# Kernel optimization log

Hardware: AMD Instinct MI355X
Metric: run time of the kernel (lower is better)

The kernel has to match this reference:

```python
import jax, jax.numpy as jnp
import numpy as np

N = 100000   # graph nodes (TSP edges)
E = 600000   # graph edges
IN_DIM = 2; HID = 128; HEADS = 16; DH = HID // HEADS
L = 4; FF = 2 * HID; OUT = 1
EPS = 1e-5; SLOPE = 0.2  # BatchNorm eps, GAT leaky_relu slope


def _mlp(x, W1, b1, W2, b2):
    return jnp.maximum(x @ W1 + b1, 0.0) @ W2 + b2


def _bn(x, g, b):
    # BatchNorm1d in training mode: batch (node-dim) statistics, biased variance
    mu = x.mean(0)
    var = x.var(0)
    return (x - mu) * jax.lax.rsqrt(var + EPS) * g + b


def _gat(h, src, dst, W, al, ar, bias):
    # DGL GATConv: per-head projection, additive attention, edge softmax over incoming edges
    z = (h @ W).reshape(N, HEADS, DH)          # [N,H,Dh]
    el = (z * al).sum(-1)                      # [N,H] source term
    er = (z * ar).sum(-1)                      # [N,H] dest term
    e = jax.nn.leaky_relu(el[src] + er[dst], SLOPE)            # [E,H]
    m = jax.ops.segment_max(e, dst, num_segments=N)            # [N,H]
    a = jnp.exp(e - m[dst])                                    # [E,H]
    denom = jax.ops.segment_sum(a, dst, num_segments=N)        # [N,H]
    msg = jax.ops.segment_sum(a[:, :, None] * z[src], dst, num_segments=N)  # [N,H,Dh]
    out = msg / jnp.where(denom > 0, denom, 1.0)[:, :, None]
    return out.reshape(N, HID) + bias


def _forward(x, src, dst,
             emb_W1, emb_b1, emb_W2, emb_b2, emb_Ws, emb_bs,
             gat_W, gat_al, gat_ar, gat_b, bn1_g, bn1_b,
             ff_W1, ff_b1, ff_W2, ff_b2, bn2_g, bn2_b,
             dec_W1, dec_b1, dec_W2, dec_b2):
    # embed MLP with skip connection
    h = _mlp(x, emb_W1, emb_b1, emb_W2, emb_b2) + (x @ emb_Ws + emb_bs)
    xs = [h]
    for l in range(L):  # fixed small layer count
        a = _gat(h, src, dst, gat_W[l], gat_al[l], gat_ar[l], gat_b[l])
        h = _bn(h + a, bn1_g[l], bn1_b[l])
        f = _mlp(h, ff_W1[l], ff_b1[l], ff_W2[l], ff_b2[l])
        h = _bn(h + f, bn2_g[l], bn2_b[l])
        xs.append(h)
    hc = jnp.concatenate(xs, axis=-1)  # JumpingKnowledge 'cat' -> [N, HID*(L+1)]
    return _mlp(hc, dec_W1, dec_b1, dec_W2, dec_b2)


def setup_inputs() -> dict:
    key = jax.random.key(0)
    ks = jax.random.split(key, 20)
    w = lambda k, shape: jax.random.normal(k, shape, jnp.float32) * 0.05
    x = jax.random.normal(ks[0], (N, IN_DIM), jnp.float32)
    src = jax.random.randint(ks[1], (E,), 0, N)
    # guarantee every node has at least one incoming edge
    dst = jnp.concatenate([jnp.arange(N), jax.random.randint(ks[2], (E - N,), 0, N)])
    return {
        'x': x, 'src': src, 'dst': dst,
        'emb_W1': w(ks[3], (IN_DIM, HID)), 'emb_b1': jnp.zeros((HID,), jnp.float32),
        'emb_W2': w(ks[4], (HID, HID)),    'emb_b2': jnp.zeros((HID,), jnp.float32),
        'emb_Ws': w(ks[5], (IN_DIM, HID)), 'emb_bs': jnp.zeros((HID,), jnp.float32),
        'gat_W': w(ks[6], (L, HID, HID)),
        'gat_al': w(ks[7], (L, HEADS, DH)), 'gat_ar': w(ks[8], (L, HEADS, DH)),
        'gat_b': jnp.zeros((L, HID), jnp.float32),
        'bn1_g': jnp.ones((L, HID), jnp.float32), 'bn1_b': jnp.zeros((L, HID), jnp.float32),
        'ff_W1': w(ks[9], (L, HID, FF)),  'ff_b1': jnp.zeros((L, FF), jnp.float32),
        'ff_W2': w(ks[10], (L, FF, HID)), 'ff_b2': jnp.zeros((L, HID), jnp.float32),
        'bn2_g': jnp.ones((L, HID), jnp.float32), 'bn2_b': jnp.zeros((L, HID), jnp.float32),
        'dec_W1': w(ks[11], (HID * (L + 1), HID)), 'dec_b1': jnp.zeros((HID,), jnp.float32),
        'dec_W2': w(ks[12], (HID, OUT)),           'dec_b2': jnp.zeros((OUT,), jnp.float32),
    }


def reference(x, src, dst,
              emb_W1, emb_b1, emb_W2, emb_b2, emb_Ws, emb_bs,
              gat_W, gat_al, gat_ar, gat_b, bn1_g, bn1_b,
              ff_W1, ff_b1, ff_W2, ff_b2, bn2_g, bn2_b,
              dec_W1, dec_b1, dec_W2, dec_b2):
    return _forward(x, src, dst,
                    emb_W1, emb_b1, emb_W2, emb_b2, emb_Ws, emb_bs,
                    gat_W, gat_al, gat_ar, gat_b, bn1_g, bn1_b,
                    ff_W1, ff_b1, ff_W2, ff_b2, bn2_g, bn2_b,
                    dec_W1, dec_b1, dec_W2, dec_b2)
```

## Files before the change

### kernel.cpp

```cpp
#include <hip/hip_runtime.h>
#include <math.h>

typedef __attribute__((ext_vector_type(8))) short bf16x8;
typedef __attribute__((ext_vector_type(4))) float f32x4;

struct BN5 {
    const float* st[5];
    const float* g[5];
    const float* b[5];
    const float* stR;
    const float* gR;
    const float* bR;
    float invN;
};

static __device__ __forceinline__ short f2bf(float f) {
    unsigned u = __float_as_uint(f);
    unsigned r = (u + 0x7fffu + ((u >> 16) & 1u)) >> 16;
    return (short)r;
}
static __device__ __forceinline__ float bf2f(short s) {
    return __uint_as_float(((unsigned)(unsigned short)s) << 16);
}
static __device__ __forceinline__ float bflo(int v) { return bf2f((short)(v & 0xffff)); }
static __device__ __forceinline__ float bfhi(int v) { return bf2f((short)(((unsigned)v) >> 16)); }
static __device__ __forceinline__ int pack2(float a, float b) {
    return (int)(((unsigned)(unsigned short)f2bf(b) << 16) | (unsigned)(unsigned short)f2bf(a));
}

__global__ void zero_i32_k(int* __restrict__ p, int n) {
    int i = blockIdx.x * 256 + threadIdx.x;
    if (i < n) p[i] = 0;
}

__global__ __launch_bounds__(256) void wconv_k(const float* __restrict__ W, short* __restrict__ Wt,
                                               int K, int Nc) {
    int slice = blockIdx.y;
    const float* src = W + (size_t)slice * K * Nc;
    short* dst = Wt + (size_t)slice * K * Nc;
    int idx = blockIdx.x * 256 + threadIdx.x;
    if (idx >= K * Nc) return;
    int k = idx / Nc, n = idx - k * Nc;
    dst[(size_t)n * K + k] = f2bf(src[idx]);
}

__global__ __launch_bounds__(256) void embed_k(
    const float* __restrict__ x, const float* __restrict__ W1, const float* __restrict__ b1,
    const float* __restrict__ Ws, const float* __restrict__ bs,
    int* __restrict__ u2, int* __restrict__ h2, int Nn)
{
    int idx = blockIdx.x * 256 + threadIdx.x;
    if (idx >= Nn * 64) return;
    int n = idx >> 6, c = (idx & 63) * 2;
    float x0 = x[2*n], x1 = x[2*n+1];
    float u0 = fmaxf(fmaf(x1, W1[128+c],   fmaf(x0, W1[c],   b1[c])),   0.f);
    float u1 = fmaxf(fmaf(x1, W1[128+c+1], fmaf(x0, W1[c+1], b1[c+1])), 0.f);
    float h0 = fmaf(x1, Ws[128+c],   fmaf(x0, Ws[c],   bs[c]));
    float h1 = fmaf(x1, Ws[128+c+1], fmaf(x0, Ws[c+1], bs[c+1]));
    u2[idx] = pack2(u0, u1);
    h2[idx] = pack2(h0, h1);
}

template<int NK, int RELU, int BETA, int ELR, int STATS>
__global__ __launch_bounds__(256) void gemm2_k(
    const short* __restrict__ A0, const short* __restrict__ A1,
    const short* __restrict__ A2, const short* __restrict__ A3,
    const short* __restrict__ A4, int Astr,
    const short* __restrict__ Wt, int ldWt,
    const float* __restrict__ bias, short* __restrict__ C, const short* __restrict__ Rres,
    int Nrows, int ldC, BN5 bn,
    const float* __restrict__ al, const float* __restrict__ ar,
    float* __restrict__ elo, float* __restrict__ ero,
    float* __restrict__ statsOut)
{
    __shared__ short Bs[128][136];
    const int row0 = blockIdx.x * 128;
    const int col0 = blockIdx.y * 128;
    const int t = threadIdx.x;
    const int w = t >> 6, lane = t & 63, q = lane >> 4, m = lane & 15;

    f32x4 acc[2][8];
    #pragma unroll
    for (int rb = 0; rb < 2; ++rb)
        #pragma unroll
        for (int cb = 0; cb < 8; ++cb)
            acc[rb][cb] = (f32x4){0.f, 0.f, 0.f, 0.f};

    const short* Asrc[5] = {A0, A1, A2, A3, A4};
    int rr0 = row0 + w*32 + m;      if (rr0 > Nrows - 1) rr0 = Nrows - 1;
    int rr1 = row0 + w*32 + 16 + m; if (rr1 > Nrows - 1) rr1 = Nrows - 1;

    #pragma unroll
    for (int kh = 0; kh < NK; ++kh) {
        if (kh) __syncthreads();
        #pragma unroll
        for (int it = 0; it < 8; ++it) {
            int ci = t + it * 256;
            int r = ci >> 4, j = (ci & 15) * 8;
            *(int4*)&Bs[r][j] = *(const int4*)(Wt + (size_t)(col0 + r) * ldWt + kh * 128 + j);
        }
        const short* pa0 = Asrc[kh] + (size_t)rr0 * Astr + q * 8;
        const short* pa1 = Asrc[kh] + (size_t)rr1 * Astr + q * 8;
        bf16x8 af0[4], af1[4];
        #pragma unroll
        for (int ks = 0; ks < 4; ++ks) {
            af0[ks] = *(const bf16x8*)(pa0 + ks * 32);
            af1[ks] = *(const bf16x8*)(pa1 + ks * 32);
        }
        if (bn.st[kh]) {
            const float* st = bn.st[kh];
            const float* gg = bn.g[kh];
            const float* bb = bn.b[kh];
            #pragma unroll
            for (int ks = 0; ks < 4; ++ks) {
                #pragma unroll
                for (int e = 0; e < 8; ++e) {
                    int c = ks * 32 + q * 8 + e;
                    float mu = st[c] * bn.invN;
                    float var = st[128 + c] * bn.invN - mu * mu;
                    float sc = rsqrtf(var + 1e-5f) * gg[c];
                    float bc = bb[c] - mu * sc;
                    af0[ks][e] = f2bf(fmaf(bf2f(af0[ks][e]), sc, bc));
                    af1[ks][e] = f2bf(fmaf(bf2f(af1[ks][e]), sc, bc));
                }
            }
        }
        __syncthreads();
        #pragma unroll
        for (int ks = 0; ks < 4; ++ks) {
            bf16x8 bfr[8];
            #pragma unroll
            for (int cb = 0; cb < 8; ++cb)
                bfr[cb] = *(const bf16x8*)&Bs[cb * 16 + m][ks * 32 + q * 8];
            #pragma unroll
            for (int cb = 0; cb < 8; ++cb) {
                acc[0][cb] = __builtin_amdgcn_mfma_f32_16x16x32_bf16(af0[ks], bfr[cb], acc[0][cb], 0, 0, 0);
                acc[1][cb] = __builtin_amdgcn_mfma_f32_16x16x32_bf16(af1[ks], bfr[cb], acc[1][cb], 0, 0, 0);
            }
        }
    }

    __syncthreads();
    short* Cs = (short*)Bs;
    #pragma unroll
    for (int rb = 0; rb < 2; ++rb) {
        #pragma unroll
        for (int r = 0; r < 4; ++r) {
            int lrow = w * 32 + rb * 16 + q * 4 + r;
            #pragma unroll
            for (int cb = 0; cb < 8; ++cb) {
                float v = acc[rb][cb][r];
                if (bias) v += bias[col0 + cb * 16 + m];
                if (RELU) v = fmaxf(v, 0.f);
                Cs[lrow * 132 + cb * 16 + m] = f2bf(v);
            }
        }
    }
    __syncthreads();
    const int chunk = t & 15, rgrp = t >> 4, cb8 = chunk * 8;
    const short* Rd = Rres ? Rres : C;
    float scR[8], bbR[8];
    if (BETA) {
        if (bn.stR) {
            #pragma unroll
            for (int e = 0; e < 8; ++e) {
                int c = cb8 + e;
                float mu = bn.stR[c] * bn.invN;
                float var = bn.stR[128 + c] * bn.invN - mu * mu;
                float sc = rsqrtf(var + 1e-5f) * bn.gR[c];
                scR[e] = sc; bbR[e] = bn.bR[c] - mu * sc;
            }
        }
    }
    float sS[8], sQ[8];
    if (STATS) {
        #pragma unroll
        for (int e = 0; e < 8; ++e) { sS[e] = 0.f; sQ[e] = 0.f; }
    }
    #pragma unroll
    for (int j = 0; j < 8; ++j) {
        int r = rgrp + j * 16;
        int grow = row0 + r;
        if (grow < Nrows) {
            int2 u0 = *(const int2*)(Cs + r * 132 + cb8);
            int2 u1 = *(const int2*)(Cs + r * 132 + cb8 + 4);
            int4 cv = make_int4(u0.x, u0.y, u1.x, u1.y);
            size_t gb = (size_t)grow * ldC + col0 + cb8;
            if (BETA) {
                int4 rv = *(const int4*)(Rd + gb);
                int* cp = (int*)&cv; const int* rp = (const int*)&rv;
                #pragma unroll
                for (int e = 0; e < 4; ++e) {
                    float rlo = bflo(rp[e]), rhi = bfhi(rp[e]);
                    if (bn.stR) {
                        rlo = fmaf(rlo, scR[2*e],   bbR[2*e]);
                        rhi = fmaf(rhi, scR[2*e+1], bbR[2*e+1]);
                    }
                    cp[e] = pack2(bflo(cp[e]) + rlo, bfhi(cp[e]) + rhi);
                }
            }
            *(int4*)(C + gb) = cv;
            if (ELR) {
                const int* cp = (const int*)&cv;
                float sl = 0.f, sr = 0.f;
                #pragma unroll
                for (int e = 0; e < 4; ++e) {
                    float lo = bflo(cp[e]), hi = bfhi(cp[e]);
                    sl = fmaf(lo, al[cb8 + 2*e], sl); sl = fmaf(hi, al[cb8 + 2*e + 1], sl);
                    sr = fmaf(lo, ar[cb8 + 2*e], sr); sr = fmaf(hi, ar[cb8 + 2*e + 1], sr);
                }
                elo[(size_t)grow * 16 + chunk] = sl;
                ero[(size_t)grow * 16 + chunk] = sr;
            }
            if (STATS) {
                const int* cp = (const int*)&cv;
                #pragma unroll
                for (int e = 0; e < 4; ++e) {
                    float lo = bflo(cp[e]), hi = bfhi(cp[e]);
                    sS[2*e]   += lo; sQ[2*e]   += lo * lo;
                    sS[2*e+1] += hi; sQ[2*e+1] += hi * hi;
                }
            }
        }
    }
    if (STATS) {
        __syncthreads();
        float* fs = (float*)Bs;
        #pragma unroll
        for (int e = 0; e < 8; ++e) {
            fs[rgrp * 128 + cb8 + e]        = sS[e];
            fs[2048 + rgrp * 128 + cb8 + e] = sQ[e];
        }
        __syncthreads();
        if (t < 128) {
            float a = 0.f;
            #pragma unroll
            for (int g = 0; g < 16; ++g) a += fs[g * 128 + t];
            atomicAdd(&statsOut[t], a);
        } else {
            int c = t - 128;
            float a = 0.f;
            #pragma unroll
            for (int g = 0; g < 16; ++g) a += fs[2048 + g * 128 + c];
            atomicAdd(&statsOut[128 + c], a);
        }
    }
}

__global__ void count_k(const int* __restrict__ dst, int* __restrict__ cnt, int E) {
    int e = blockIdx.x * 256 + threadIdx.x;
    if (e < E) atomicAdd(&cnt[dst[e]], 1);
}

__global__ __launch_bounds__(256) void scan_part_k(const int* __restrict__ cnt,
                                                   int* __restrict__ bsum, int Nn) {
    __shared__ int red[256];
    int base = blockIdx.x * 1024;
    int s = 0;
    for (int i = threadIdx.x; i < 1024; i += 256) {
        int g = base + i;
        if (g < Nn) s += cnt[g];
    }
    red[threadIdx.x] = s; __syncthreads();
    for (int off = 128; off; off >>= 1) {
        if ((int)threadIdx.x < off) red[threadIdx.x] += red[threadIdx.x + off];
        __syncthreads();
    }
    if (threadIdx.x == 0) bsum[blockIdx.x] = red[0];
}

__global__ __launch_bounds__(256) void scan_top_k(int* __restrict__ bsum, int nb) {
    __shared__ int buf[256];
    int v = ((int)threadIdx.x < nb) ? bsum[threadIdx.x] : 0;
    buf[threadIdx.x] = v; __syncthreads();
    for (int off = 1; off < 256; off <<= 1) {
        int tv = ((int)threadIdx.x >= off) ? buf[threadIdx.x - off] : 0;
        __syncthreads();
        buf[threadIdx.x] += tv;
        __syncthreads();
    }
    if ((int)threadIdx.x < nb) bsum[threadIdx.x] = buf[threadIdx.x] - v;
}

__global__ __launch_bounds__(256) void scan_fin_k(const int* __restrict__ cnt,
    const int* __restrict__ bsum, int* __restrict__ rowptr, int* __restrict__ wpos, int Nn)
{
    __shared__ int tsum[256];
    int base = blockIdx.x * 1024;
    int g0 = base + (int)threadIdx.x * 4;
    int v[4]; int s = 0;
    #pragma unroll
    for (int j = 0; j < 4; ++j) {
        int g = g0 + j;
        v[j] = (g < Nn) ? cnt[g] : 0;
        s += v[j];
    }
    tsum[threadIdx.x] = s; __syncthreads();
    for (int off = 1; off < 256; off <<= 1) {
        int tv = ((int)threadIdx.x >= off) ? tsum[threadIdx.x - off] : 0;
        __syncthreads();
        tsum[threadIdx.x] += tv;
        __syncthreads();
    }
    int run = bsum[blockIdx.x] + tsum[threadIdx.x] - s;
    #pragma unroll
    for (int j = 0; j < 4; ++j) {
        int g = g0 + j;
        if (g < Nn) { wpos[g] = run; rowptr[g + 1] = run + v[j]; }
        run += v[j];
    }
    if (blockIdx.x == 0 && threadIdx.x == 0) rowptr[0] = 0;
}

__global__ void scatter_k(const int* __restrict__ src, const int* __restrict__ dst,
                          int* __restrict__ wpos, int* __restrict__ esrc, int E) {
    int e = blockIdx.x * 256 + threadIdx.x;
    if (e < E) {
        int p = atomicAdd(&wpos[dst[e]], 1);
        esrc[p] = src[e];
    }
}

__global__ __launch_bounds__(256) void gat_k(
    const short* __restrict__ h, const short* __restrict__ z,
    const float* __restrict__ el, const float* __restrict__ er,
    const int* __restrict__ rowptr, const int* __restrict__ esrc,
    const float* __restrict__ gbias, short* __restrict__ t1, int Nn,
    const float* __restrict__ hstats, const float* __restrict__ hg,
    const float* __restrict__ hb, float invN)
{
    int gw = (blockIdx.x * 256 + threadIdx.x) >> 6;
    if (gw >= Nn) return;
    int lane = threadIdx.x & 63;
    int c = lane * 2;
    int head = lane >> 2;
    float ern = er[gw*16 + head];
    int beg = rowptr[gw], end = rowptr[gw+1];
    float m = -3.0e38f, den = 0.f, a0 = 0.f, a1 = 0.f;
    int i = beg;
    for (; i + 3 < end; i += 4) {
        int s0 = esrc[i], s1 = esrc[i+1], s2 = esrc[i+2], s3 = esrc[i+3];
        float e0 = el[s0*16 + head] + ern;
        float e1 = el[s1*16 + head] + ern;
        float e2 = el[s2*16 + head] + ern;
        float e3 = el[s3*16 + head] + ern;
        int zz0 = *(const int*)(z + (size_t)s0*128 + c);
        int zz1 = *(const int*)(z + (size_t)s1*128 + c);
        int zz2 = *(const int*)(z + (size_t)s2*128 + c);
        int zz3 = *(const int*)(z + (size_t)s3*128 + c);
        e0 = (e0 > 0.f) ? e0 : 0.2f * e0;
        e1 = (e1 > 0.f) ? e1 : 0.2f * e1;
        e2 = (e2 > 0.f) ? e2 : 0.2f * e2;
        e3 = (e3 > 0.f) ? e3 : 0.2f * e3;
        float nm = fmaxf(fmaxf(fmaxf(e0, e1), fmaxf(e2, e3)), m);
        float sc = __expf(m - nm);
        float w0 = __expf(e0 - nm), w1 = __expf(e1 - nm);
        float w2 = __expf(e2 - nm), w3 = __expf(e3 - nm);
        den = fmaf(den, sc, (w0 + w1) + (w2 + w3));
        a0 = fmaf(a0, sc, fmaf(w0, bflo(zz0), fmaf(w1, bflo(zz1), fmaf(w2, bflo(zz2), w3 * bflo(zz3)))));
        a1 = fmaf(a1, sc, fmaf(w0, bfhi(zz0), fmaf(w1, bfhi(zz1), fmaf(w2, bfhi(zz2), w3 * bfhi(zz3)))));
        m = nm;
    }
    for (; i + 1 < end; i += 2) {
        int s0 = esrc[i], s1 = esrc[i+1];
        float e0 = el[s0*16 + head] + ern;
        float e1 = el[s1*16 + head] + ern;
        int zz0 = *(const int*)(z + (size_t)s0*128 + c);
        int zz1 = *(const int*)(z + (size_t)s1*128 + c);
        e0 = (e0 > 0.f) ? e0 : 0.2f * e0;
        e1 = (e1 > 0.f) ? e1 : 0.2f * e1;
        float nm = fmaxf(m, fmaxf(e0, e1));
        float sc = __expf(m - nm);
        float w0 = __expf(e0 - nm);
        float w1 = __expf(e1 - nm);
        den = fmaf(den, sc, w0 + w1);
        a0  = fmaf(a0, sc, fmaf(w0, bflo(zz0), w1 * bflo(zz1)));
        a1  = fmaf(a1, sc, fmaf(w0, bfhi(zz0), w1 * bfhi(zz1)));
        m = nm;
    }
    if (i < end) {
        int s0 = esrc[i];
        float e0 = el[s0*16 + head] + ern;
        int zz0 = *(const int*)(z + (size_t)s0*128 + c);
        e0 = (e0 > 0.f) ? e0 : 0.2f * e0;
        float nm = fmaxf(m, e0);
        float sc = __expf(m - nm);
        float w0 = __expf(e0 - nm);
        den = fmaf(den, sc, w0);
        a0  = fmaf(a0, sc, w0 * bflo(zz0));
        a1  = fmaf(a1, sc, w0 * bfhi(zz0));
    }
    float inv = 1.f / den;
    size_t o = (size_t)gw*64 + lane;
    int hv = ((const int*)h)[o];
    float h0 = bflo(hv), h1 = bfhi(hv);
    if (hstats) {
        float mu0 = hstats[c] * invN;
        float v0  = hstats[128+c] * invN - mu0*mu0;
        float s0  = rsqrtf(v0 + 1e-5f) * hg[c];
        h0 = fmaf(h0 - mu0, s0, hb[c]);
        float mu1 = hstats[c+1] * invN;
        float v1  = hstats[128+c+1] * invN - mu1*mu1;
        float s1  = rsqrtf(v1 + 1e-5f) * hg[c+1];
        h1 = fmaf(h1 - mu1, s1, hb[c+1]);
    }
    float r0 = h0 + a0*inv + gbias[c];
    float r1 = h1 + a1*inv + gbias[c+1];
    ((int*)t1)[o] = pack2(r0, r1);
}

__global__ __launch_bounds__(256) void bn_stats_k(const short* __restrict__ xin,
    float* __restrict__ stats, int Nn)
{
    __shared__ float s0s[256], s1s[256], q0s[256], q1s[256];
    int pair = threadIdx.x & 63;
    int slot = threadIdx.x >> 6;
    float s0 = 0.f, s1 = 0.f, q0 = 0.f, q1 = 0.f;
    for (int r = blockIdx.x*4 + slot; r < Nn; r += gridDim.x*4) {
        int v = *(const int*)(xin + (size_t)r*128 + pair*2);
        float a = bflo(v), b = bfhi(v);
        s0 += a; s1 += b;
        q0 = fmaf(a, a, q0); q1 = fmaf(b, b, q1);
    }
    s0s[threadIdx.x] = s0; s1s[threadIdx.x] = s1;
    q0s[threadIdx.x] = q0; q1s[threadIdx.x] = q1;
    __syncthreads();
    if (slot == 0) {
        #pragma unroll
        for (int j = 1; j < 4; ++j) {
            s0 += s0s[pair + j*64]; s1 += s1s[pair + j*64];
            q0 += q0s[pair + j*64]; q1 += q1s[pair + j*64];
        }
        atomicAdd(&stats[pair*2],       s0);
        atomicAdd(&stats[pair*2+1],     s1);
        atomicAdd(&stats[128+pair*2],   q0);
        atomicAdd(&stats[128+pair*2+1], q1);
    }
}

__global__ __launch_bounds__(256) void dec_out_k(const short* __restrict__ udec,
    const float* __restrict__ W2, const float* __restrict__ b2,
    float* __restrict__ out, int Nn)
{
    int gw = (blockIdx.x * 256 + threadIdx.x) >> 6;
    if (gw >= Nn) return;
    int lane = threadIdx.x & 63;
    int v = ((const int*)(udec + (size_t)gw * 128))[lane];
    float p = bflo(v) * W2[lane*2] + bfhi(v) * W2[lane*2 + 1];
    #pragma unroll
    for (int off = 32; off > 0; off >>= 1) p += __shfl_down(p, off);
    if (lane == 0) out[gw] = p + b2[0];
}

extern "C" void kernel_launch(void* const* d_in, const int* in_sizes, int n_in,
                              void* d_out, int out_size, void* d_ws, size_t ws_size,
                              hipStream_t stream)
{
    const float* x      = (const float*)d_in[0];
    const int*   src    = (const int*)  d_in[1];
    const int*   dst    = (const int*)  d_in[2];
    const float* emb_W1 = (const float*)d_in[3];
    const float* emb_b1 = (const float*)d_in[4];
    const float* emb_W2 = (const float*)d_in[5];
    const float* emb_b2 = (const float*)d_in[6];
    const float* emb_Ws = (const float*)d_in[7];
    const float* emb_bs = (const float*)d_in[8];
    const float* gat_W  = (const float*)d_in[9];
    const float* gat_al = (const float*)d_in[10];
    const float* gat_ar = (const float*)d_in[11];
    const float* gat_b  = (const float*)d_in[12];
    const float* bn1_g  = (const float*)d_in[13];
    const float* bn1_b  = (const float*)d_in[14];
    const float* ff_W1  = (const float*)d_in[15];
    const float* ff_b1  = (const float*)d_in[16];
    const float* ff_W2  = (const float*)d_in[17];
    const float* ff_b2  = (const float*)d_in[18];
    const float* bn2_g  = (const float*)d_in[19];
    const float* bn2_b  = (const float*)d_in[20];
    const float* dec_W1 = (const float*)d_in[21];
    const float* dec_b1 = (const float*)d_in[22];
    const float* dec_W2 = (const float*)d_in[23];
    const float* dec_b2 = (const float*)d_in[24];
    float* out = (float*)d_out;
    (void)n_in; (void)out_size;

    const int N = in_sizes[0] / 2;
    const int E = in_sizes[1];
    const float invN = 1.f / (float)N;

    char* p = (char*)d_ws;
    size_t used = 0;
    auto carve = [&](size_t bytes) {
        char* r = p; size_t a = (bytes + 255) & ~(size_t)255;
        p += a; used += a; return r;
    };
    const size_t nbH = (size_t)N * 128 * 2;
    short* xs[5];
    for (int i = 0; i < 5; ++i) xs[i] = (short*)carve(nbH);
    short* t1   = (short*)carve(nbH);
    char*  big  = (char*)carve(2 * nbH);
    int*   cnt    = (int*)carve((size_t)N * 4);
    float* stats8 = (float*)carve(8 * 256 * 4);
    int*   rowptr = (int*)carve((size_t)(N + 1) * 4);
    int*   wpos   = (int*)carve((size_t)N * 4);
    int*   esrc   = (int*)carve((size_t)E * 4);
    int*   bsum   = (int*)carve(256 * 4);
    short* emb_W2t = (short*)carve((size_t)128 * 128 * 2);
    short* gat_Wt  = (short*)carve((size_t)4 * 128 * 128 * 2);
    short* ff_W1t  = (short*)carve((size_t)4 * 128 * 256 * 2);
    short* ff_W2t  = (short*)carve((size_t)4 * 256 * 128 * 2);
    short* dec_W1t = (short*)carve((size_t)640 * 128 * 2);
    if (used > ws_size) return;

    short* u    = (short*)big;
    short* z    = (short*)big;
    float* el   = (float*)(big + nbH);
    float* er   = el + (size_t)N * 16;
    short* ffh  = (short*)big;
    short* udec = (short*)big;

    dim3 b256(256);
    int ecb  = (E + 255) / 256;
    int nel2 = (N * 64 + 255) / 256;
    int gx   = (N + 127) / 128;
    int nwv  = (N + 3) / 4;
    int nb   = (N + 1023) / 1024;

    BN5 bn0;
    for (int i = 0; i < 5; ++i) { bn0.st[i] = nullptr; bn0.g[i] = nullptr; bn0.b[i] = nullptr; }
    bn0.stR = nullptr; bn0.gR = nullptr; bn0.bR = nullptr; bn0.invN = invN;

    wconv_k<<<dim3(64, 1), b256, 0, stream>>>(emb_W2, emb_W2t, 128, 128);
    wconv_k<<<dim3(64, 4), b256, 0, stream>>>(gat_W,  gat_Wt,  128, 128);
    wconv_k<<<dim3(128, 4), b256, 0, stream>>>(ff_W1, ff_W1t,  128, 256);
    wconv_k<<<dim3(128, 4), b256, 0, stream>>>(ff_W2, ff_W2t,  256, 128);
    wconv_k<<<dim3(320, 1), b256, 0, stream>>>(dec_W1, dec_W1t, 640, 128);

    {
        int ztot = (int)(((char*)(stats8 + 8*256) - (char*)cnt) / 4);
        zero_i32_k<<<(ztot + 255) / 256, b256, 0, stream>>>(cnt, ztot);
    }

    count_k<<<ecb, b256, 0, stream>>>(dst, cnt, E);
    scan_part_k<<<nb, b256, 0, stream>>>(cnt, bsum, N);
    scan_top_k<<<1, b256, 0, stream>>>(bsum, nb);
    scan_fin_k<<<nb, b256, 0, stream>>>(cnt, bsum, rowptr, wpos, N);
    scatter_k<<<ecb, b256, 0, stream>>>(src, dst, wpos, esrc, E);

    embed_k<<<nel2, b256, 0, stream>>>(x, emb_W1, emb_b1, emb_Ws, emb_bs, (int*)u, (int*)xs[0], N);
    gemm2_k<1,0,1,0,0><<<dim3(gx,1), b256, 0, stream>>>(u,u,u,u,u, 128, emb_W2t, 128,
        emb_b2, xs[0], nullptr, N, 128, bn0, nullptr, nullptr, nullptr, nullptr, nullptr);

    for (int l = 0; l < 4; ++l) {
        float* st1 = stats8 + (size_t)(l*2)   * 256;
        float* st2 = stats8 + (size_t)(l*2+1) * 256;
        short* hl = xs[l];
        const float* hst = (l == 0) ? nullptr : stats8 + (size_t)((l-1)*2+1) * 256;
        const float* hgp = (l == 0) ? nullptr : bn2_g + (l-1)*128;
        const float* hbp = (l == 0) ? nullptr : bn2_b + (l-1)*128;

        BN5 bz = bn0; bz.st[0] = hst; bz.g[0] = hgp; bz.b[0] = hbp;
        gemm2_k<1,0,0,1,0><<<dim3(gx,1), b256, 0, stream>>>(hl,hl,hl,hl,hl, 128,
            gat_Wt + (size_t)l*128*128, 128, nullptr, z, nullptr, N, 128, bz,
            gat_al + l*128, gat_ar + l*128, el, er, nullptr);
        gat_k<<<nwv, b256, 0, stream>>>(hl, z, el, er, rowptr, esrc, gat_b + l*128, t1, N,
                                        hst, hgp, hbp, invN);
        bn_stats_k<<<400, b256, 0, stream>>>(t1, st1, N);
        BN5 bf1 = bn0; bf1.st[0] = st1; bf1.g[0] = bn1_g + l*128; bf1.b[0] = bn1_b + l*128;
        gemm2_k<1,1,0,0,0><<<dim3(gx,2), b256, 0, stream>>>(t1,t1,t1,t1,t1, 128,
            ff_W1t + (size_t)l*128*256, 128, ff_b1 + l*256, ffh, nullptr, N, 256, bf1,
            nullptr, nullptr, nullptr, nullptr, nullptr);
        BN5 bf2 = bn0; bf2.stR = st1; bf2.gR = bn1_g + l*128; bf2.bR = bn1_b + l*128;
        gemm2_k<2,0,1,0,1><<<dim3(gx,1), b256, 0, stream>>>(ffh, ffh + 128, ffh, ffh, ffh, 256,
            ff_W2t + (size_t)l*256*128, 256, ff_b2 + l*128, xs[l+1], t1, N, 128, bf2,
            nullptr, nullptr, nullptr, nullptr, st2);
    }

    BN5 bd = bn0;
    for (int k = 1; k < 5; ++k) {
        bd.st[k] = stats8 + (size_t)((k-1)*2+1) * 256;
        bd.g[k]  = bn2_g + (k-1)*128;
        bd.b[k]  = bn2_b + (k-1)*128;
    }
    gemm2_k<5,1,0,0,0><<<dim3(gx,1), b256, 0, stream>>>(xs[0], xs[1], xs[2], xs[3], xs[4], 128,
        dec_W1t, 640, dec_b1, udec, nullptr, N, 128, bd,
        nullptr, nullptr, nullptr, nullptr, nullptr);
    dec_out_k<<<nwv, b256, 0, stream>>>(udec, dec_W2, dec_b2, out, N);
}
```

Measured before the change: 1.146 ms.

## Fuse feed-forward MLP GEMMs into one kernel keeping hidden activations in LDS

Replaces the two FF GEMM launches per layer with a single kernel. It applies BN1 to the input rows, computes the 256-wide ReLU hidden layer in two 128-column halves held in shared memory, and accumulates the second GEMM directly. The residual add, BN2 statistics and output store move into the same epilogue. This drops the N×256 bf16 hidden-activation round trip through global memory and one launch per layer. In exchange it uses more shared memory per block, holds more accumulator registers and adds extra syncthreads, which may lower occupancy.

New measurement: 1.062 ms. -7.4%, faster.

```diff
diff --git a/kernel.cpp b/kernel.cpp
--- a/kernel.cpp
+++ b/kernel.cpp
@@ -61,7 +61,7 @@
     h2[idx] = pack2(h0, h1);
 }
 
-template<int NK, int RELU, int BETA, int ELR, int STATS>
+template<int NK, int RELU, int BETA, int ELR>
 __global__ __launch_bounds__(256) void gemm2_k(
     const short* __restrict__ A0, const short* __restrict__ A1,
     const short* __restrict__ A2, const short* __restrict__ A3,
@@ -70,8 +70,7 @@
     const float* __restrict__ bias, short* __restrict__ C, const short* __restrict__ Rres,
     int Nrows, int ldC, BN5 bn,
     const float* __restrict__ al, const float* __restrict__ ar,
-    float* __restrict__ elo, float* __restrict__ ero,
-    float* __restrict__ statsOut)
+    float* __restrict__ elo, float* __restrict__ ero)
 {
     __shared__ short Bs[128][136];
     const int row0 = blockIdx.x * 128;
@@ -159,24 +158,6 @@
     __syncthreads();
     const int chunk = t & 15, rgrp = t >> 4, cb8 = chunk * 8;
     const short* Rd = Rres ? Rres : C;
-    float scR[8], bbR[8];
-    if (BETA) {
-        if (bn.stR) {
-            #pragma unroll
-            for (int e = 0; e < 8; ++e) {
-                int c = cb8 + e;
-                float mu = bn.stR[c] * bn.invN;
-                float var = bn.stR[128 + c] * bn.invN - mu * mu;
-                float sc = rsqrtf(var + 1e-5f) * bn.gR[c];
-                scR[e] = sc; bbR[e] = bn.bR[c] - mu * sc;
-            }
-        }
-    }
-    float sS[8], sQ[8];
-    if (STATS) {
-        #pragma unroll
-        for (int e = 0; e < 8; ++e) { sS[e] = 0.f; sQ[e] = 0.f; }
-    }
     #pragma unroll
     for (int j = 0; j < 8; ++j) {
         int r = rgrp + j * 16;
@@ -190,14 +171,8 @@
                 int4 rv = *(const int4*)(Rd + gb);
                 int* cp = (int*)&cv; const int* rp = (const int*)&rv;
                 #pragma unroll
-                for (int e = 0; e < 4; ++e) {
-                    float rlo = bflo(rp[e]), rhi = bfhi(rp[e]);
-                    if (bn.stR) {
-                        rlo = fmaf(rlo, scR[2*e],   bbR[2*e]);
-                        rhi = fmaf(rhi, scR[2*e+1], bbR[2*e+1]);
-                    }
-                    cp[e] = pack2(bflo(cp[e]) + rlo, bfhi(cp[e]) + rhi);
-                }
+                for (int e = 0; e < 4; ++e)
+                    cp[e] = pack2(bflo(cp[e]) + bflo(rp[e]), bfhi(cp[e]) + bfhi(rp[e]));
             }
             *(int4*)(C + gb) = cv;
             if (ELR) {
@@ -212,38 +187,195 @@
                 elo[(size_t)grow * 16 + chunk] = sl;
                 ero[(size_t)grow * 16 + chunk] = sr;
             }
-            if (STATS) {
-                const int* cp = (const int*)&cv;
+        }
+    }
+}
+
+__global__ __launch_bounds__(256) void ff_fused_k(
+    const short* __restrict__ T1,
+    const short* __restrict__ W1t,
+    const short* __restrict__ W2t,
+    const float* __restrict__ b1, const float* __restrict__ b2,
+    const float* __restrict__ st1, const float* __restrict__ g1, const float* __restrict__ bb1,
+    float invN, short* __restrict__ C, int Nrows, float* __restrict__ statsOut)
+{
+    __shared__ short Wbuf[128][136];
+    __shared__ short Fbuf[128 * 132];
+    const int row0 = blockIdx.x * 128;
+    const int t = threadIdx.x;
+    const int w = t >> 6, lane = t & 63, q = lane >> 4, m = lane & 15;
+
+    f32x4 acc2[2][8];
+    #pragma unroll
+    for (int rb = 0; rb < 2; ++rb)
+        #pragma unroll
+        for (int cb = 0; cb < 8; ++cb)
+            acc2[rb][cb] = (f32x4){0.f, 0.f, 0.f, 0.f};
+
+    int rr0 = row0 + w*32 + m;      if (rr0 > Nrows - 1) rr0 = Nrows - 1;
+    int rr1 = row0 + w*32 + 16 + m; if (rr1 > Nrows - 1) rr1 = Nrows - 1;
+
+    bf16x8 af0[4], af1[4];
+    {
+        const short* pa0 = T1 + (size_t)rr0 * 128 + q * 8;
+        const short* pa1 = T1 + (size_t)rr1 * 128 + q * 8;
+        #pragma unroll
+        for (int ks = 0; ks < 4; ++ks) {
+            af0[ks] = *(const bf16x8*)(pa0 + ks * 32);
+            af1[ks] = *(const bf16x8*)(pa1 + ks * 32);
+        }
+        #pragma unroll
+        for (int ks = 0; ks < 4; ++ks) {
+            #pragma unroll
+            for (int e = 0; e < 8; ++e) {
+                int c = ks * 32 + q * 8 + e;
+                float mu = st1[c] * invN;
+                float var = st1[128 + c] * invN - mu * mu;
+                float sc = rsqrtf(var + 1e-5f) * g1[c];
+                float bc = bb1[c] - mu * sc;
+                af0[ks][e] = f2bf(fmaf(bf2f(af0[ks][e]), sc, bc));
+                af1[ks][e] = f2bf(fmaf(bf2f(af1[ks][e]), sc, bc));
+            }
+        }
+    }
+
+    #pragma unroll
+    for (int half = 0; half < 2; ++half) {
+        if (half) __syncthreads();
+        #pragma unroll
+        for (int it = 0; it < 8; ++it) {
+            int ci = t + it * 256;
+            int r = ci >> 4, j = (ci & 15) * 8;
+            *(int4*)&Wbuf[r][j] = *(const int4*)(W1t + (size_t)(half * 128 + r) * 128 + j);
+        }
+        __syncthreads();
+        f32x4 acc1[2][8];
+        #pragma unroll
+        for (int rb = 0; rb < 2; ++rb)
+            #pragma unroll
+            for (int cb = 0; cb < 8; ++cb)
+                acc1[rb][cb] = (f32x4){0.f, 0.f, 0.f, 0.f};
+        #pragma unroll
+        for (int ks = 0; ks < 4; ++ks) {
+            bf16x8 bfr[8];
+            #pragma unroll
+            for (int cb = 0; cb < 8; ++cb)
+                bfr[cb] = *(const bf16x8*)&Wbuf[cb * 16 + m][ks * 32 + q * 8];
+            #pragma unroll
+            for (int cb = 0; cb < 8; ++cb) {
+                acc1[0][cb] = __builtin_amdgcn_mfma_f32_16x16x32_bf16(af0[ks], bfr[cb], acc1[0][cb], 0, 0, 0);
+                acc1[1][cb] = __builtin_amdgcn_mfma_f32_16x16x32_bf16(af1[ks], bfr[cb], acc1[1][cb], 0, 0, 0);
+            }
+        }
+        #pragma unroll
+        for (int rb = 0; rb < 2; ++rb) {
+            #pragma unroll
+            for (int r = 0; r < 4; ++r) {
+                int lrow = w * 32 + rb * 16 + q * 4 + r;
                 #pragma unroll
-                for (int e = 0; e < 4; ++e) {
-                    float lo = bflo(cp[e]), hi = bfhi(cp[e]);
-                    sS[2*e]   += lo; sQ[2*e]   += lo * lo;
-                    sS[2*e+1] += hi; sQ[2*e+1] += hi * hi;
+                for (int cb = 0; cb < 8; ++cb) {
+                    float v = acc1[rb][cb][r] + b1[half * 128 + cb * 16 + m];
+                    Fbuf[lrow * 132 + cb * 16 + m] = f2bf(fmaxf(v, 0.f));
                 }
             }
         }
-    }
-    if (STATS) {
-        __syncthreads();
-        float* fs = (float*)Bs;
-        #pragma unroll
-        for (int e = 0; e < 8; ++e) {
-            fs[rgrp * 128 + cb8 + e]        = sS[e];
-            fs[2048 + rgrp * 128 + cb8 + e] = sQ[e];
-        }
-        __syncthreads();
-        if (t < 128) {
-            float a = 0.f;
-            #pragma unroll
-            for (int g = 0; g < 16; ++g) a += fs[g * 128 + t];
-            atomicAdd(&statsOut[t], a);
-        } else {
-            int c = t - 128;
-            float a = 0.f;
-            #pragma unroll
-            for (int g = 0; g < 16; ++g) a += fs[2048 + g * 128 + c];
-            atomicAdd(&statsOut[128 + c], a);
-        }
+        __syncthreads();
+        #pragma unroll
+        for (int it = 0; it < 8; ++it) {
+            int ci = t + it * 256;
+            int r = ci >> 4, j = (ci & 15) * 8;
+            *(int4*)&Wbuf[r][j] = *(const int4*)(W2t + (size_t)r * 256 + half * 128 + j);
+        }
+        __syncthreads();
+        const short* fa0 = Fbuf + (w * 32 + m) * 132 + q * 8;
+        const short* fa1 = Fbuf + (w * 32 + 16 + m) * 132 + q * 8;
+        #pragma unroll
+        for (int ks = 0; ks < 4; ++ks) {
+            bf16x8 ga0 = *(const bf16x8*)(fa0 + ks * 32);
+            bf16x8 ga1 = *(const bf16x8*)(fa1 + ks * 32);
+            bf16x8 bfr[8];
+            #pragma unroll
+            for (int cb = 0; cb < 8; ++cb)
+                bfr[cb] = *(const bf16x8*)&Wbuf[cb * 16 + m][ks * 32 + q * 8];
+            #pragma unroll
+            for (int cb = 0; cb < 8; ++cb) {
+                acc2[0][cb] = __builtin_amdgcn_mfma_f32_16x16x32_bf16(ga0, bfr[cb], acc2[0][cb], 0, 0, 0);
+                acc2[1][cb] = __builtin_amdgcn_mfma_f32_16x16x32_bf16(ga1, bfr[cb], acc2[1][cb], 0, 0, 0);
+            }
+        }
+    }
+
+    __syncthreads();
+    #pragma unroll
+    for (int rb = 0; rb < 2; ++rb) {
+        #pragma unroll
+        for (int r = 0; r < 4; ++r) {
+            int lrow = w * 32 + rb * 16 + q * 4 + r;
+            #pragma unroll
+            for (int cb = 0; cb < 8; ++cb) {
+                float v = acc2[rb][cb][r] + b2[cb * 16 + m];
+                Fbuf[lrow * 132 + cb * 16 + m] = f2bf(v);
+            }
+        }
+    }
+    __syncthreads();
+    const int chunk = t & 15, rgrp = t >> 4, cb8 = chunk * 8;
+    float scR[8], bbR[8];
+    #pragma unroll
+    for (int e = 0; e < 8; ++e) {
+        int c = cb8 + e;
+        float mu = st1[c] * invN;
+        float var = st1[128 + c] * invN - mu * mu;
+        float sc = rsqrtf(var + 1e-5f) * g1[c];
+        scR[e] = sc; bbR[e] = bb1[c] - mu * sc;
+    }
+    float sS[8], sQ[8];
+    #pragma unroll
+    for (int e = 0; e < 8; ++e) { sS[e] = 0.f; sQ[e] = 0.f; }
+    #pragma unroll
+    for (int j = 0; j < 8; ++j) {
+        int r = rgrp + j * 16;
+        int grow = row0 + r;
+        if (grow < Nrows) {
+            int2 u0 = *(const int2*)(Fbuf + r * 132 + cb8);
+            int2 u1 = *(const int2*)(Fbuf + r * 132 + cb8 + 4);
+            int4 cv = make_int4(u0.x, u0.y, u1.x, u1.y);
+            size_t gb = (size_t)grow * 128 + cb8;
+            int4 rv = *(const int4*)(T1 + gb);
+            int* cp = (int*)&cv; const int* rp = (const int*)&rv;
+            #pragma unroll
+            for (int e = 0; e < 4; ++e) {
+                float rlo = fmaf(bflo(rp[e]), scR[2*e],   bbR[2*e]);
+                float rhi = fmaf(bfhi(rp[e]), scR[2*e+1], bbR[2*e+1]);
+                float lo = bflo(cp[e]) + rlo;
+                float hi = bfhi(cp[e]) + rhi;
+                cp[e] = pack2(lo, hi);
+                lo = bflo(cp[e]); hi = bfhi(cp[e]);
+                sS[2*e]   += lo; sQ[2*e]   += lo * lo;
+                sS[2*e+1] += hi; sQ[2*e+1] += hi * hi;
+            }
+            *(int4*)(C + gb) = cv;
+        }
+    }
+    __syncthreads();
+    float* fs = (float*)Wbuf;
+    #pragma unroll
+    for (int e = 0; e < 8; ++e) {
+        fs[rgrp * 128 + cb8 + e]        = sS[e];
+        fs[2048 + rgrp * 128 + cb8 + e] = sQ[e];
+    }
+    __syncthreads();
+    if (t < 128) {
+        float a = 0.f;
+        #pragma unroll
+        for (int g = 0; g < 16; ++g) a += fs[g * 128 + t];
+        atomicAdd(&statsOut[t], a);
+    } else {
+        int c = t - 128;
+        float a = 0.f;
+        #pragma unroll
+        for (int g = 0; g < 16; ++g) a += fs[2048 + g * 128 + c];
+        atomicAdd(&statsOut[128 + c], a);
     }
 }
 
@@ -516,7 +648,6 @@
     short* z    = (short*)big;
     float* el   = (float*)(big + nbH);
     float* er   = el + (size_t)N * 16;
-    short* ffh  = (short*)big;
     short* udec = (short*)big;
 
     dim3 b256(256);
@@ -548,8 +679,8 @@
     scatter_k<<<ecb, b256, 0, stream>>>(src, dst, wpos, esrc, E);
 
     embed_k<<<nel2, b256, 0, stream>>>(x, emb_W1, emb_b1, emb_Ws, emb_bs, (int*)u, (int*)xs[0], N);
-    gemm2_k<1,0,1,0,0><<<dim3(gx,1), b256, 0, stream>>>(u,u,u,u,u, 128, emb_W2t, 128,
-        emb_b2, xs[0], nullptr, N, 128, bn0, nullptr, nullptr, nullptr, nullptr, nullptr);
+    gemm2_k<1,0,1,0><<<dim3(gx,1), b256, 0, stream>>>(u,u,u,u,u, 128, emb_W2t, 128,
+        emb_b2, xs[0], nullptr, N, 128, bn0, nullptr, nullptr, nullptr, nullptr);
 
     for (int l = 0; l < 4; ++l) {
         float* st1 = stats8 + (size_t)(l*2)   * 256;
@@ -560,20 +691,17 @@
         const float* hbp = (l == 0) ? nullptr : bn2_b + (l-1)*128;
 
         BN5 bz = bn0; bz.st[0] = hst; bz.g[0] = hgp; bz.b[0] = hbp;
-        gemm2_k<1,0,0,1,0><<<dim3(gx,1), b256, 0, stream>>>(hl,hl,hl,hl,hl, 128,
+        gemm2_k<1,0,0,1><<<dim3(gx,1), b256, 0, stream>>>(hl,hl,hl,hl,hl, 128,
             gat_Wt + (size_t)l*128*128, 128, nullptr, z, nullptr, N, 128, bz,
-            gat_al + l*128, gat_ar + l*128, el, er, nullptr);
+            gat_al + l*128, gat_ar + l*128, el, er);
         gat_k<<<nwv, b256, 0, stream>>>(hl, z, el, er, rowptr, esrc, gat_b + l*128, t1, N,
                                         hst, hgp, hbp, invN);
         bn_stats_k<<<400, b256, 0, stream>>>(t1, st1, N);
-        BN5 bf1 = bn0; bf1.st[0] = st1; bf1.g[0] = bn1_g + l*128; bf1.b[0] = bn1_b + l*128;
-        gemm2_k<1,1,0,0,0><<<dim3(gx,2), b256, 0, stream>>>(t1,t1,t1,t1,t1, 128,
-            ff_W1t + (size_t)l*128*256, 128, ff_b1 + l*256, ffh, nullptr, N, 256, bf1,
-            nullptr, nullptr, nullptr, nullptr, nullptr);
-        BN5 bf2 = bn0; bf2.stR = st1; bf2.gR = bn1_g + l*128; bf2.bR = bn1_b + l*128;
-        gemm2_k<2,0,1,0,1><<<dim3(gx,1), b256, 0, stream>>>(ffh, ffh + 128, ffh, ffh, ffh, 256,
-            ff_W2t + (size_t)l*256*128, 256, ff_b2 + l*128, xs[l+1], t1, N, 128, bf2,
-            nullptr, nullptr, nullptr, nullptr, st2);
+        ff_fused_k<<<gx, b256, 0, stream>>>(t1,
+            ff_W1t + (size_t)l*128*256, ff_W2t + (size_t)l*256*128,
+            ff_b1 + l*256, ff_b2 + l*128,
+            st1, bn1_g + l*128, bn1_b + l*128, invN,
+            xs[l+1], N, st2);
     }
 
     BN5 bd = bn0;
@@ -582,8 +710,8 @@
         bd.g[k]  = bn2_g + (k-1)*128;
         bd.b[k]  = bn2_b + (k-1)*128;
     }
-    gemm2_k<5,1,0,0,0><<<dim3(gx,1), b256, 0, stream>>>(xs[0], xs[1], xs[2], xs[3], xs[4], 128,
+    gemm2_k<5,1,0,0><<<dim3(gx,1), b256, 0, stream>>>(xs[0], xs[1], xs[2], xs[3], xs[4], 128,
         dec_W1t, 640, dec_b1, udec, nullptr, N, 128, bd,
-        nullptr, nullptr, nullptr, nullptr, nullptr);
+        nullptr, nullptr, nullptr, nullptr);
     dec_out_k<<<nwv, b256, 0, stream>>>(udec, dec_W2, dec_b2, out, N);
 }
```
